# Optimization experiments

Hardware: AMD Instinct MI355X
Metric: run time of the kernel (lower is better)

## Reference

```python
import jax, jax.numpy as jnp
import numpy as np

D_MODEL = 1024
H = 16
D = D_MODEL // H  # 64 per-head dim
B, T = 2, 2048


def setup_inputs() -> dict:
    key = jax.random.key(0)
    ks = jax.random.split(key, 5)
    scale = 1.0 / np.sqrt(D_MODEL)
    x = jax.random.normal(ks[0], (B, T, D_MODEL), dtype=jnp.float32)
    Wqkv = jax.random.normal(ks[1], (D_MODEL, 3 * D_MODEL), dtype=jnp.float32) * scale
    bqkv = jnp.zeros((3 * D_MODEL,), dtype=jnp.float32)
    Wproj = jax.random.normal(ks[2], (D_MODEL, D_MODEL), dtype=jnp.float32) * scale
    bproj = jnp.zeros((D_MODEL,), dtype=jnp.float32)
    return {"x": x, "Wqkv": Wqkv, "bqkv": bqkv, "Wproj": Wproj, "bproj": bproj}


def reference(x, Wqkv, bqkv, Wproj, bproj):
    b, t, d_model = x.shape
    h, d = H, D
    qkv = x @ Wqkv + bqkv  # [b, t, 3*d_model]
    q, k, v = jnp.split(qkv, 3, axis=-1)
    # [b, t, d_model] -> [b, h, t, d]
    q = q.reshape(b, t, h, d).transpose(0, 2, 1, 3)
    k = k.reshape(b, t, h, d).transpose(0, 2, 1, 3)
    v = v.reshape(b, t, h, d).transpose(0, 2, 1, 3)
    att = jnp.einsum('bhqd,bhkd->bhqk', q, k) / jnp.sqrt(jnp.float32(d))
    causal = jnp.tril(jnp.ones((t, t), dtype=bool))  # [t, t]
    att = jnp.where(causal[None, None, :, :], att, -jnp.inf)
    att = jax.nn.softmax(att, axis=-1)
    # dropout in eval mode -> identity (deterministic reference)
    out = jnp.einsum('bhqk,bhkd->bhqd', att, v)  # [b, h, t, d]
    out = out.transpose(0, 2, 1, 3).reshape(b, t, d_model)
    out = out @ Wproj + bproj
    return out
```

## Files before the change

### kernel.cpp

```cpp
#include <hip/hip_runtime.h>
#include <cstddef>

typedef __bf16 bf16x8 __attribute__((ext_vector_type(8)));
typedef float  f32x4  __attribute__((ext_vector_type(4)));

__device__ __forceinline__ float bf2f(unsigned short s) {
    return __uint_as_float(((unsigned int)s) << 16);
}
__device__ __forceinline__ unsigned short f2bf(float x) {
    unsigned int u = __float_as_uint(x);
    unsigned int r = u + 0x7fffu + ((u >> 16) & 1u);
    return (unsigned short)(r >> 16);
}

__device__ __forceinline__ void async_load16(const void* g, void* l) {
    __builtin_amdgcn_global_load_lds(
        (const __attribute__((address_space(1))) unsigned int*)g,
        (__attribute__((address_space(3))) unsigned int*)l,
        16, 0, 0);
}

__global__ __launch_bounds__(256) void prep_kernel(
    const void* __restrict__ x, const void* __restrict__ Wqkv,
    const void* __restrict__ Wproj,
    unsigned short* __restrict__ xb, unsigned short* __restrict__ WqkvT,
    unsigned short* __restrict__ WprojT, int* __restrict__ flagp)
{
    __shared__ unsigned short T[64][72];
    __shared__ int cnt;
    const int tid = threadIdx.x;
    const int bid = blockIdx.x;

    if (tid == 0) cnt = 0;
    __syncthreads();
    {
        unsigned short u = ((const unsigned short*)x)[tid << 1];
        int e = (u >> 7) & 0xFF;
        int wild = ((e >= 0x90) || (e >= 1 && e <= 0x48)) ? 1 : 0;
        unsigned long long ball = __ballot(wild);
        if ((tid & 63) == 0) atomicAdd(&cnt, (int)__popcll(ball));
    }
    __syncthreads();
    const bool f32 = (cnt > 64);
    if (bid == 0 && tid == 0) *flagp = f32 ? 1 : 0;

    if (bid < 2048) {
        const size_t off = ((size_t)bid * 256 + tid) * 8;
        if (f32) {
            const float* s = (const float*)x + off;
            float4 a = *(const float4*)s;
            float4 b = *(const float4*)(s + 4);
            uint4 o;
            o.x = (unsigned)f2bf(a.x) | ((unsigned)f2bf(a.y) << 16);
            o.y = (unsigned)f2bf(a.z) | ((unsigned)f2bf(a.w) << 16);
            o.z = (unsigned)f2bf(b.x) | ((unsigned)f2bf(b.y) << 16);
            o.w = (unsigned)f2bf(b.z) | ((unsigned)f2bf(b.w) << 16);
            *(uint4*)(xb + off) = o;
        } else {
            *(uint4*)(xb + off) = *(const uint4*)((const unsigned short*)x + off);
        }
        return;
    }

    const void* src; unsigned short* dst; int C, bx, by;
    if (bid < 2048 + 768) {
        const int t2 = bid - 2048;
        src = Wqkv; dst = WqkvT; C = 3072;
        bx = t2 % 48; by = t2 / 48;
    } else {
        const int t2 = bid - 2816;
        src = Wproj; dst = WprojT; C = 1024;
        bx = t2 % 16; by = t2 / 16;
    }
    const int R = 1024;
    const int c0 = bx * 64, r0 = by * 64;
    const int r  = tid >> 2, cl = (tid & 3) << 4;

    unsigned short v[16];
    if (f32) {
        const float* s = (const float*)src + (size_t)(r0 + r) * C + c0 + cl;
        #pragma unroll
        for (int q = 0; q < 4; ++q) {
            float4 a = *(const float4*)(s + q * 4);
            v[q * 4 + 0] = f2bf(a.x); v[q * 4 + 1] = f2bf(a.y);
            v[q * 4 + 2] = f2bf(a.z); v[q * 4 + 3] = f2bf(a.w);
        }
    } else {
        const unsigned short* s = (const unsigned short*)src + (size_t)(r0 + r) * C + c0 + cl;
        uint4 a = *(const uint4*)s;
        uint4 b = *(const uint4*)(s + 8);
        unsigned int w[8] = {a.x, a.y, a.z, a.w, b.x, b.y, b.z, b.w};
        #pragma unroll
        for (int q = 0; q < 8; ++q) {
            v[q * 2]     = (unsigned short)(w[q] & 0xffffu);
            v[q * 2 + 1] = (unsigned short)(w[q] >> 16);
        }
    }
    #pragma unroll
    for (int c = 0; c < 16; ++c) T[cl + c][r] = v[c];
    __syncthreads();

    const int c = tid >> 2, rl = (tid & 3) << 4;
    uint4 o0 = *(const uint4*)&T[c][rl];
    uint4 o1 = *(const uint4*)&T[c][rl + 8];
    unsigned short* dp = dst + (size_t)(c0 + c) * R + r0 + rl;
    *(uint4*)dp       = o0;
    *(uint4*)(dp + 8) = o1;
}

__device__ __forceinline__ void bt_mainloop(
    const unsigned short* __restrict__ A,
    const unsigned short* __restrict__ BT,
    int K, int m0, int n0,
    unsigned short* As, unsigned short* Bs,
    f32x4 (&acc)[4][4])
{
    const int tid  = threadIdx.x;
    const int wave = tid >> 6;
    const int lane = tid & 63;
    const int mrow = lane & 15;
    const int quad = lane >> 4;
    const int wr = wave >> 1, wc = wave & 1;
    const int srow = tid >> 2;
    const int scol = (tid & 3) << 3;

    const unsigned short* ga  = A  + (size_t)(m0 + srow) * K + scol;
    const unsigned short* ga2 = ga + (size_t)64 * K;
    const unsigned short* gb  = BT + (size_t)(n0 + srow) * K + scol;
    const unsigned short* gb2 = gb + (size_t)64 * K;
    unsigned short* lA  = As + wave * 512;
    unsigned short* lA2 = As + 2048 + wave * 512;
    unsigned short* lB  = Bs + wave * 512;
    unsigned short* lB2 = Bs + 2048 + wave * 512;

    for (int k0 = 0; k0 < K; k0 += 32) {
        async_load16(ga,  lA);
        async_load16(ga2, lA2);
        async_load16(gb,  lB);
        async_load16(gb2, lB2);
        ga += 32; ga2 += 32; gb += 32; gb2 += 32;
        __syncthreads();

        bf16x8 afr[4], bfr[4];
        #pragma unroll
        for (int mt = 0; mt < 4; ++mt)
            afr[mt] = *(const bf16x8*)(As + (wr * 64 + mt * 16 + mrow) * 32 + quad * 8);
        #pragma unroll
        for (int nt = 0; nt < 4; ++nt)
            bfr[nt] = *(const bf16x8*)(Bs + (wc * 64 + nt * 16 + mrow) * 32 + quad * 8);
        #pragma unroll
        for (int mt = 0; mt < 4; ++mt) {
            #pragma unroll
            for (int nt = 0; nt < 4; ++nt)
                acc[mt][nt] = __builtin_amdgcn_mfma_f32_16x16x32_bf16(
                    afr[mt], bfr[nt], acc[mt][nt], 0, 0, 0);
        }
        __syncthreads();
    }
}

__global__ __launch_bounds__(256) void gemm_qkv_bt(
    const int* __restrict__ flag,
    const unsigned short* __restrict__ A,
    const unsigned short* __restrict__ BT,
    const void* __restrict__ bias,
    unsigned short* __restrict__ Qb, unsigned short* __restrict__ Kb,
    unsigned short* __restrict__ VbT)
{
    __shared__ unsigned short As[128 * 32];
    __shared__ unsigned short Bs[128 * 32];
    const int m0 = blockIdx.y * 128, n0 = blockIdx.x * 128;

    f32x4 acc[4][4];
    #pragma unroll
    for (int mt = 0; mt < 4; ++mt)
        #pragma unroll
        for (int nt = 0; nt < 4; ++nt)
            { acc[mt][nt][0]=0.f; acc[mt][nt][1]=0.f; acc[mt][nt][2]=0.f; acc[mt][nt][3]=0.f; }

    bt_mainloop(A, BT, 1024, m0, n0, As, Bs, acc);

    const int tid  = threadIdx.x;
    const int wave = tid >> 6;
    const int lane = tid & 63;
    const int mrow = lane & 15;
    const int quad = lane >> 4;
    const int wr = wave >> 1, wc = wave & 1;
    const bool f32b = (*flag != 0);

    #pragma unroll
    for (int nt = 0; nt < 4; ++nt) {
        const int n = n0 + wc * 64 + nt * 16 + mrow;
        const float bv = f32b ? ((const float*)bias)[n]
                              : bf2f(((const unsigned short*)bias)[n]);
        const int sel = n >> 10;
        const int h   = (n & 1023) >> 6;
        const int d   = n & 63;
        const float sc = (sel == 0) ? 0.125f : 1.0f;
        #pragma unroll
        for (int mt = 0; mt < 4; ++mt) {
            #pragma unroll
            for (int r = 0; r < 4; ++r) {
                const int m  = m0 + wr * 64 + mt * 16 + quad * 4 + r;
                const int bb = m >> 11;
                const int t  = m & 2047;
                const unsigned short ov = f2bf((acc[mt][nt][r] + bv) * sc);
                const int bhh = bb * 16 + h;
                if (sel == 0)      Qb [(((size_t)bhh * 2048 + t) << 6) + d] = ov;
                else if (sel == 1) Kb [(((size_t)bhh * 2048 + t) << 6) + d] = ov;
                else               VbT[((((size_t)bhh << 6) + d) << 11) + t] = ov;
            }
        }
    }
}

__global__ __launch_bounds__(256) void gemm_proj_n64(
    const int* __restrict__ flag,
    const unsigned short* __restrict__ A,
    const unsigned short* __restrict__ BT,
    const void* __restrict__ bias, void* __restrict__ Out)
{
    __shared__ unsigned short As[128 * 32];
    __shared__ unsigned short Bs[64 * 32];
    const int K = 1024;
    const int m0 = blockIdx.y * 128, n0 = blockIdx.x * 64;

    const int tid  = threadIdx.x;
    const int wave = tid >> 6;
    const int lane = tid & 63;
    const int mrow = lane & 15;
    const int quad = lane >> 4;
    const int wr = wave >> 1, wc = wave & 1;
    const int srow = tid >> 2;
    const int scol = (tid & 3) << 3;

    f32x4 acc[4][2];
    #pragma unroll
    for (int mt = 0; mt < 4; ++mt)
        #pragma unroll
        for (int nt = 0; nt < 2; ++nt)
            { acc[mt][nt][0]=0.f; acc[mt][nt][1]=0.f; acc[mt][nt][2]=0.f; acc[mt][nt][3]=0.f; }

    const unsigned short* ga  = A  + (size_t)(m0 + srow) * K + scol;
    const unsigned short* ga2 = ga + (size_t)64 * K;
    const unsigned short* gb  = BT + (size_t)(n0 + srow) * K + scol;
    unsigned short* lA  = As + wave * 512;
    unsigned short* lA2 = As + 2048 + wave * 512;
    unsigned short* lB  = Bs + wave * 512;

    for (int k0 = 0; k0 < K; k0 += 32) {
        async_load16(ga,  lA);
        async_load16(ga2, lA2);
        async_load16(gb,  lB);
        ga += 32; ga2 += 32; gb += 32;
        __syncthreads();

        bf16x8 afr[4], bfr[2];
        #pragma unroll
        for (int mt = 0; mt < 4; ++mt)
            afr[mt] = *(const bf16x8*)(As + (wr * 64 + mt * 16 + mrow) * 32 + quad * 8);
        #pragma unroll
        for (int nt = 0; nt < 2; ++nt)
            bfr[nt] = *(const bf16x8*)(Bs + (wc * 32 + nt * 16 + mrow) * 32 + quad * 8);
        #pragma unroll
        for (int mt = 0; mt < 4; ++mt) {
            #pragma unroll
            for (int nt = 0; nt < 2; ++nt)
                acc[mt][nt] = __builtin_amdgcn_mfma_f32_16x16x32_bf16(
                    afr[mt], bfr[nt], acc[mt][nt], 0, 0, 0);
        }
        __syncthreads();
    }

    const bool f32b = (*flag != 0);
    #pragma unroll
    for (int nt = 0; nt < 2; ++nt) {
        const int n = n0 + wc * 32 + nt * 16 + mrow;
        const float bv = f32b ? ((const float*)bias)[n]
                              : bf2f(((const unsigned short*)bias)[n]);
        #pragma unroll
        for (int mt = 0; mt < 4; ++mt) {
            #pragma unroll
            for (int r = 0; r < 4; ++r) {
                const int m = m0 + wr * 64 + mt * 16 + quad * 4 + r;
                const float val = acc[mt][nt][r] + bv;
                if (f32b) ((float*)Out)[(size_t)m * 1024 + n] = val;
                else      ((unsigned short*)Out)[(size_t)m * 1024 + n] = f2bf(val);
            }
        }
    }
}

__global__ __launch_bounds__(256) void attn_kernel(
    const unsigned short* __restrict__ Qb,
    const unsigned short* __restrict__ Kb,
    const unsigned short* __restrict__ VbT,
    unsigned short* __restrict__ Attn)
{
    __shared__ unsigned short Ks2[2][2][64 * 32];
    __shared__ unsigned short Vs2[2][2][64 * 32];
    __shared__ unsigned short Ps[64][72];

    const int tid  = threadIdx.x;
    const int wave = tid >> 6;
    const int lane = tid & 63;
    const int mrow = lane & 15;
    const int quad = lane >> 4;

    const int blk   = blockIdx.x;
    const int xcd   = blk & 7;
    const int slot  = blk >> 3;
    const int bh    = (xcd << 2) | (slot & 3);
    const int qpair = slot >> 2;
    const int b     = bh >> 4, h = bh & 15;

    const int krow  = tid >> 2;
    const int kcol8 = (tid & 3) << 3;

    const unsigned short* Qbase = Qb  + ((size_t)bh << 17);
    const unsigned short* Kbase = Kb  + ((size_t)bh << 17);
    const unsigned short* Vtb   = VbT + ((size_t)bh << 17);

    bf16x8 ones;
    #pragma unroll
    for (int e = 0; e < 8; ++e) ones[e] = (__bf16)1.0f;

    for (int half = 0; half < 2; ++half) {
        const int qblk = (half == 0) ? qpair : (31 - qpair);
        const int q0   = qblk << 6;
        const int nr   = qblk + 1;

        bf16x8 aq[2];
        {
            const unsigned short* qp = Qbase + (size_t)(q0 + wave * 16 + mrow) * 64 + quad * 8;
            aq[0] = *(const bf16x8*)qp;
            aq[1] = *(const bf16x8*)(qp + 32);
        }

        f32x4 Oa[4];
        #pragma unroll
        for (int dt = 0; dt < 4; ++dt) { Oa[dt][0]=0.f; Oa[dt][1]=0.f; Oa[dt][2]=0.f; Oa[dt][3]=0.f; }
        f32x4 la; la[0]=0.f; la[1]=0.f; la[2]=0.f; la[3]=0.f;

        __syncthreads();
        {
            #pragma unroll
            for (int h2 = 0; h2 < 2; ++h2)
                async_load16(Kbase + (size_t)krow * 64 + h2 * 32 + kcol8,
                             &Ks2[0][h2][krow * 32 + kcol8]);
            #pragma unroll
            for (int j2 = 0; j2 < 2; ++j2)
                async_load16(Vtb + ((size_t)krow << 11) + j2 * 32 + kcol8,
                             &Vs2[0][j2][krow * 32 + kcol8]);
        }

        for (int rr = 0; rr < nr; ++rr) {
            __syncthreads();

            if (rr + 1 < nr) {
                const int nt0 = (rr + 1) << 6;
                const int nb  = (rr + 1) & 1;
                #pragma unroll
                for (int h2 = 0; h2 < 2; ++h2)
                    async_load16(Kbase + (size_t)(nt0 + krow) * 64 + h2 * 32 + kcol8,
                                 &Ks2[nb][h2][krow * 32 + kcol8]);
                #pragma unroll
                for (int j2 = 0; j2 < 2; ++j2)
                    async_load16(Vtb + ((size_t)krow << 11) + nt0 + j2 * 32 + kcol8,
                                 &Vs2[nb][j2][krow * 32 + kcol8]);
            }

            const int cb  = rr & 1;
            const int kt0 = rr << 6;

            f32x4 sacc[4];
            #pragma unroll
            for (int jt = 0; jt < 4; ++jt) { sacc[jt][0]=0.f; sacc[jt][1]=0.f; sacc[jt][2]=0.f; sacc[jt][3]=0.f; }
            #pragma unroll
            for (int ks = 0; ks < 2; ++ks) {
                #pragma unroll
                for (int jt = 0; jt < 4; ++jt) {
                    bf16x8 bk = *(const bf16x8*)&Ks2[cb][ks][(jt * 16 + mrow) * 32 + quad * 8];
                    sacc[jt] = __builtin_amdgcn_mfma_f32_16x16x32_bf16(aq[ks], bk, sacc[jt], 0, 0, 0);
                }
            }

            if (rr == nr - 1) {
                #pragma unroll
                for (int jt = 0; jt < 4; ++jt) {
                    const int jg = kt0 + jt * 16 + mrow;
                    #pragma unroll
                    for (int r = 0; r < 4; ++r) {
                        if (jg > q0 + wave * 16 + quad * 4 + r) sacc[jt][r] = -1e30f;
                    }
                }
            }

            #pragma unroll
            for (int jt = 0; jt < 4; ++jt) {
                #pragma unroll
                for (int r = 0; r < 4; ++r) {
                    const float pv = __expf(sacc[jt][r] - 16.0f);
                    Ps[wave * 16 + quad * 4 + r][jt * 16 + mrow] = f2bf(pv);
                }
            }

            __threadfence_block();

            #pragma unroll
            for (int ks2 = 0; ks2 < 2; ++ks2) {
                bf16x8 ap = *(const bf16x8*)&Ps[wave * 16 + mrow][ks2 * 32 + quad * 8];
                la = __builtin_amdgcn_mfma_f32_16x16x32_bf16(ap, ones, la, 0, 0, 0);
                #pragma unroll
                for (int dt = 0; dt < 4; ++dt) {
                    bf16x8 bv = *(const bf16x8*)&Vs2[cb][ks2][(dt * 16 + mrow) * 32 + quad * 8];
                    Oa[dt] = __builtin_amdgcn_mfma_f32_16x16x32_bf16(ap, bv, Oa[dt], 0, 0, 0);
                }
            }
        }

        #pragma unroll
        for (int r = 0; r < 4; ++r) {
            const float inv = 1.0f / la[r];
            const int t = q0 + wave * 16 + quad * 4 + r;
            const size_t base = ((size_t)(b * 2048 + t)) * 1024 + h * 64;
            #pragma unroll
            for (int dt = 0; dt < 4; ++dt)
                Attn[base + dt * 16 + mrow] = f2bf(Oa[dt][r] * inv);
        }
    }
}

extern "C" void kernel_launch(void* const* d_in, const int* in_sizes, int n_in,
                              void* d_out, int out_size, void* d_ws, size_t ws_size,
                              hipStream_t stream)
{
    const void* x     = d_in[0];
    const void* Wqkv  = d_in[1];
    const void* bqkv  = d_in[2];
    const void* Wproj = d_in[3];
    const void* bproj = d_in[4];

    int* flag = (int*)d_ws;
    unsigned short* ws = (unsigned short*)d_ws;
    unsigned short* xb     = ws + 64;
    unsigned short* shared = xb + 4194304;
    unsigned short* WqkvT  = shared;
    unsigned short* Attn   = shared;
    unsigned short* WprojT = shared + 4194304;
    unsigned short* Qb     = WprojT + 1048576;
    unsigned short* Kb     = Qb + 4194304;
    unsigned short* VbT    = Kb + 4194304;

    prep_kernel<<<3072, 256, 0, stream>>>(x, Wqkv, Wproj, xb, WqkvT, WprojT, flag);
    gemm_qkv_bt<<<dim3(24, 32), 256, 0, stream>>>(flag, xb, WqkvT, bqkv, Qb, Kb, VbT);
    attn_kernel<<<512, 256, 0, stream>>>(Qb, Kb, VbT, Attn);
    gemm_proj_n64<<<dim3(16, 32), 256, 0, stream>>>(flag, Attn, WprojT, bproj, d_out);
}
```

Before: 190.9 us.

## Split attention into one q-block per workgroup with swizzled LDS layouts

The attention kernel now launches one workgroup per 64-row query block instead of pairing two blocks in a loop, so the grid doubles to 1024 blocks. A new schedule maps block indices so the heaviest causal blocks are dispatched first. K/V tiles and the P scratch buffer switch from padded or linear layouts to XOR-swizzled layouts to avoid LDS bank conflicts. The cost is that the balancing from pairing short and long rows is lost and Q loads and setup are repeated per block.

```diff
diff --git a/kernel.cpp b/kernel.cpp
--- a/kernel.cpp
+++ b/kernel.cpp
@@ -299,7 +299,7 @@
 {
     __shared__ unsigned short Ks2[2][2][64 * 32];
     __shared__ unsigned short Vs2[2][2][64 * 32];
-    __shared__ unsigned short Ps[64][72];
+    __shared__ unsigned short Ps[64 * 64];
 
     const int tid  = threadIdx.x;
     const int wave = tid >> 6;
@@ -307,15 +307,26 @@
     const int mrow = lane & 15;
     const int quad = lane >> 4;
 
-    const int blk   = blockIdx.x;
-    const int xcd   = blk & 7;
-    const int slot  = blk >> 3;
-    const int bh    = (xcd << 2) | (slot & 3);
-    const int qpair = slot >> 2;
-    const int b     = bh >> 4, h = bh & 15;
-
-    const int krow  = tid >> 2;
-    const int kcol8 = (tid & 3) << 3;
+    const int blk  = blockIdx.x;
+    const int xcd  = blk & 7;
+    const int j    = blk >> 3;
+    const int s    = j >> 5;
+    const int w    = j & 31;
+    const int t8   = w >> 2;
+    const int bh   = (xcd << 2) | (w & 3);
+    const int qblk = (s == 0) ? 31 - t8 : (s == 1) ? 23 - t8
+                   : (s == 2) ? 8 + t8   : t8;
+    const int q0   = qblk << 6;
+    const int nr   = qblk + 1;
+    const int b    = bh >> 4, h = bh & 15;
+
+    const int lc    = tid & 63;
+    const int sc_   = lc ^ ((lc >> 3) & 7);
+    const int grow  = wave * 16 + (sc_ >> 2);
+    const int gcol8 = (sc_ & 3) << 3;
+    const int ldst  = tid * 8;
+
+    const int swzro = ((mrow * 4 + quad) ^ ((mrow >> 1) & 7)) << 3;
 
     const unsigned short* Qbase = Qb  + ((size_t)bh << 17);
     const unsigned short* Kbase = Kb  + ((size_t)bh << 17);
@@ -325,109 +336,103 @@
     #pragma unroll
     for (int e = 0; e < 8; ++e) ones[e] = (__bf16)1.0f;
 
-    for (int half = 0; half < 2; ++half) {
-        const int qblk = (half == 0) ? qpair : (31 - qpair);
-        const int q0   = qblk << 6;
-        const int nr   = qblk + 1;
-
-        bf16x8 aq[2];
-        {
-            const unsigned short* qp = Qbase + (size_t)(q0 + wave * 16 + mrow) * 64 + quad * 8;
-            aq[0] = *(const bf16x8*)qp;
-            aq[1] = *(const bf16x8*)(qp + 32);
-        }
-
-        f32x4 Oa[4];
-        #pragma unroll
-        for (int dt = 0; dt < 4; ++dt) { Oa[dt][0]=0.f; Oa[dt][1]=0.f; Oa[dt][2]=0.f; Oa[dt][3]=0.f; }
-        f32x4 la; la[0]=0.f; la[1]=0.f; la[2]=0.f; la[3]=0.f;
-
+    bf16x8 aq[2];
+    {
+        const unsigned short* qp = Qbase + (size_t)(q0 + wave * 16 + mrow) * 64 + quad * 8;
+        aq[0] = *(const bf16x8*)qp;
+        aq[1] = *(const bf16x8*)(qp + 32);
+    }
+
+    f32x4 Oa[4];
+    #pragma unroll
+    for (int dt = 0; dt < 4; ++dt) { Oa[dt][0]=0.f; Oa[dt][1]=0.f; Oa[dt][2]=0.f; Oa[dt][3]=0.f; }
+    f32x4 la; la[0]=0.f; la[1]=0.f; la[2]=0.f; la[3]=0.f;
+
+    #pragma unroll
+    for (int h2 = 0; h2 < 2; ++h2)
+        async_load16(Kbase + (size_t)grow * 64 + h2 * 32 + gcol8,
+                     &Ks2[0][h2][ldst]);
+    #pragma unroll
+    for (int j2 = 0; j2 < 2; ++j2)
+        async_load16(Vtb + ((size_t)grow << 11) + j2 * 32 + gcol8,
+                     &Vs2[0][j2][ldst]);
+
+    for (int rr = 0; rr < nr; ++rr) {
         __syncthreads();
-        {
+
+        if (rr + 1 < nr) {
+            const int nt0 = (rr + 1) << 6;
+            const int nb  = (rr + 1) & 1;
             #pragma unroll
             for (int h2 = 0; h2 < 2; ++h2)
-                async_load16(Kbase + (size_t)krow * 64 + h2 * 32 + kcol8,
-                             &Ks2[0][h2][krow * 32 + kcol8]);
+                async_load16(Kbase + (size_t)(nt0 + grow) * 64 + h2 * 32 + gcol8,
+                             &Ks2[nb][h2][ldst]);
             #pragma unroll
             for (int j2 = 0; j2 < 2; ++j2)
-                async_load16(Vtb + ((size_t)krow << 11) + j2 * 32 + kcol8,
-                             &Vs2[0][j2][krow * 32 + kcol8]);
-        }
-
-        for (int rr = 0; rr < nr; ++rr) {
-            __syncthreads();
-
-            if (rr + 1 < nr) {
-                const int nt0 = (rr + 1) << 6;
-                const int nb  = (rr + 1) & 1;
-                #pragma unroll
-                for (int h2 = 0; h2 < 2; ++h2)
-                    async_load16(Kbase + (size_t)(nt0 + krow) * 64 + h2 * 32 + kcol8,
-                                 &Ks2[nb][h2][krow * 32 + kcol8]);
-                #pragma unroll
-                for (int j2 = 0; j2 < 2; ++j2)
-                    async_load16(Vtb + ((size_t)krow << 11) + nt0 + j2 * 32 + kcol8,
-                                 &Vs2[nb][j2][krow * 32 + kcol8]);
-            }
-
-            const int cb  = rr & 1;
-            const int kt0 = rr << 6;
-
-            f32x4 sacc[4];
-            #pragma unroll
-            for (int jt = 0; jt < 4; ++jt) { sacc[jt][0]=0.f; sacc[jt][1]=0.f; sacc[jt][2]=0.f; sacc[jt][3]=0.f; }
-            #pragma unroll
-            for (int ks = 0; ks < 2; ++ks) {
-                #pragma unroll
-                for (int jt = 0; jt < 4; ++jt) {
-                    bf16x8 bk = *(const bf16x8*)&Ks2[cb][ks][(jt * 16 + mrow) * 32 + quad * 8];
-                    sacc[jt] = __builtin_amdgcn_mfma_f32_16x16x32_bf16(aq[ks], bk, sacc[jt], 0, 0, 0);
-                }
-            }
-
-            if (rr == nr - 1) {
-                #pragma unroll
-                for (int jt = 0; jt < 4; ++jt) {
-                    const int jg = kt0 + jt * 16 + mrow;
-                    #pragma unroll
-                    for (int r = 0; r < 4; ++r) {
-                        if (jg > q0 + wave * 16 + quad * 4 + r) sacc[jt][r] = -1e30f;
-                    }
-                }
-            }
-
+                async_load16(Vtb + ((size_t)grow << 11) + nt0 + j2 * 32 + gcol8,
+                             &Vs2[nb][j2][ldst]);
+        }
+
+        const int cb  = rr & 1;
+        const int kt0 = rr << 6;
+
+        f32x4 sacc[4];
+        #pragma unroll
+        for (int jt = 0; jt < 4; ++jt) { sacc[jt][0]=0.f; sacc[jt][1]=0.f; sacc[jt][2]=0.f; sacc[jt][3]=0.f; }
+        #pragma unroll
+        for (int ks = 0; ks < 2; ++ks) {
             #pragma unroll
             for (int jt = 0; jt < 4; ++jt) {
+                bf16x8 bk = *(const bf16x8*)&Ks2[cb][ks][jt * 512 + swzro];
+                sacc[jt] = __builtin_amdgcn_mfma_f32_16x16x32_bf16(aq[ks], bk, sacc[jt], 0, 0, 0);
+            }
+        }
+
+        if (rr == nr - 1) {
+            #pragma unroll
+            for (int jt = 0; jt < 4; ++jt) {
+                const int jg = kt0 + jt * 16 + mrow;
                 #pragma unroll
                 for (int r = 0; r < 4; ++r) {
-                    const float pv = __expf(sacc[jt][r] - 16.0f);
-                    Ps[wave * 16 + quad * 4 + r][jt * 16 + mrow] = f2bf(pv);
+                    if (jg > q0 + wave * 16 + quad * 4 + r) sacc[jt][r] = -1e30f;
                 }
             }
-
-            __threadfence_block();
-
-            #pragma unroll
-            for (int ks2 = 0; ks2 < 2; ++ks2) {
-                bf16x8 ap = *(const bf16x8*)&Ps[wave * 16 + mrow][ks2 * 32 + quad * 8];
-                la = __builtin_amdgcn_mfma_f32_16x16x32_bf16(ap, ones, la, 0, 0, 0);
-                #pragma unroll
-                for (int dt = 0; dt < 4; ++dt) {
-                    bf16x8 bv = *(const bf16x8*)&Vs2[cb][ks2][(dt * 16 + mrow) * 32 + quad * 8];
-                    Oa[dt] = __builtin_amdgcn_mfma_f32_16x16x32_bf16(ap, bv, Oa[dt], 0, 0, 0);
-                }
-            }
-        }
-
-        #pragma unroll
-        for (int r = 0; r < 4; ++r) {
-            const float inv = 1.0f / la[r];
-            const int t = q0 + wave * 16 + quad * 4 + r;
-            const size_t base = ((size_t)(b * 2048 + t)) * 1024 + h * 64;
-            #pragma unroll
-            for (int dt = 0; dt < 4; ++dt)
-                Attn[base + dt * 16 + mrow] = f2bf(Oa[dt][r] * inv);
-        }
+        }
+
+        #pragma unroll
+        for (int jt = 0; jt < 4; ++jt) {
+            #pragma unroll
+            for (int r = 0; r < 4; ++r) {
+                const float pv = __expf(sacc[jt][r] - 16.0f);
+                const int row = wave * 16 + quad * 4 + r;
+                const int col = jt * 16 + mrow;
+                Ps[row * 64 + ((((col >> 3) ^ (row & 7)) << 3) | (col & 7))] = f2bf(pv);
+            }
+        }
+
+        __threadfence_block();
+
+        const int prow = wave * 16 + mrow;
+        #pragma unroll
+        for (int ks2 = 0; ks2 < 2; ++ks2) {
+            bf16x8 ap = *(const bf16x8*)&Ps[prow * 64 + (((ks2 * 4 + quad) ^ (mrow & 7)) << 3)];
+            la = __builtin_amdgcn_mfma_f32_16x16x32_bf16(ap, ones, la, 0, 0, 0);
+            #pragma unroll
+            for (int dt = 0; dt < 4; ++dt) {
+                bf16x8 bv = *(const bf16x8*)&Vs2[cb][ks2][dt * 512 + swzro];
+                Oa[dt] = __builtin_amdgcn_mfma_f32_16x16x32_bf16(ap, bv, Oa[dt], 0, 0, 0);
+            }
+        }
+    }
+
+    #pragma unroll
+    for (int r = 0; r < 4; ++r) {
+        const float inv = 1.0f / la[r];
+        const int t = q0 + wave * 16 + quad * 4 + r;
+        const size_t base = ((size_t)(b * 2048 + t)) * 1024 + h * 64;
+        #pragma unroll
+        for (int dt = 0; dt < 4; ++dt)
+            Attn[base + dt * 16 + mrow] = f2bf(Oa[dt][r] * inv);
     }
 }
 
@@ -454,6 +459,6 @@
 
     prep_kernel<<<3072, 256, 0, stream>>>(x, Wqkv, Wproj, xb, WqkvT, WprojT, flag);
     gemm_qkv_bt<<<dim3(24, 32), 256, 0, stream>>>(flag, xb, WqkvT, bqkv, Qb, Kb, VbT);
-    attn_kernel<<<512, 256, 0, stream>>>(Qb, Kb, VbT, Attn);
+    attn_kernel<<<1024, 256, 0, stream>>>(Qb, Kb, VbT, Attn);
     gemm_proj_n64<<<dim3(16, 32), 256, 0, stream>>>(flag, Attn, WprojT, bproj, d_out);
 }
```

Result: no change. 187.5 us (-1.8%).
